# Optimization experiments

Hardware: AMD Instinct MI355X
Metric: run time of the kernel (lower is better)

## Reference

```python
import jax, jax.numpy as jnp
import numpy as np

B, D, L = 32, 512, 4096   # batch, latent_dim (dim1), time length
N, D2 = 77, 768           # text tokens, text_latent_dim (dim2)
BC = 24                   # number of conditioned batch elements
H = 8                     # num_heads
EPS = 1e-5


def _layernorm(x, g, b):
    mu = jnp.mean(x, axis=-1, keepdims=True)
    var = jnp.mean(jnp.square(x - mu), axis=-1, keepdims=True)
    return (x - mu) * jax.lax.rsqrt(var + EPS) * g + b


def setup_inputs() -> dict:
    key = jax.random.key(0)
    ks = jax.random.split(key, 8)
    s = 0.02
    return {
        "input_tensor": jax.random.normal(ks[0], (B, D, L), jnp.float32),
        "condition_tensor": jax.random.normal(ks[1], (B, N, D2), jnp.float32),
        "cond_indices": jnp.arange(BC, dtype=jnp.int64 if jax.config.jax_enable_x64 else jnp.int32),
        "ln_g": jnp.ones((D,), jnp.float32),
        "ln_b": jnp.zeros((D,), jnp.float32),
        "tln_g": jnp.ones((D2,), jnp.float32),
        "tln_b": jnp.zeros((D2,), jnp.float32),
        "Wq": jax.random.normal(ks[2], (D, D), jnp.float32) * s,
        "bq": jnp.zeros((D,), jnp.float32),
        "Wk": jax.random.normal(ks[3], (D2, D), jnp.float32) * s,
        "bk": jnp.zeros((D,), jnp.float32),
        "Wv": jax.random.normal(ks[4], (D2, D), jnp.float32) * s,
        "bv": jnp.zeros((D,), jnp.float32),
    }


def reference(input_tensor, condition_tensor, cond_indices,
              ln_g, ln_b, tln_g, tln_b, Wq, bq, Wk, bk, Wv, bv):
    dh = D // H
    # gather conditioned rows; [Bc, D, L] -> [Bc, T=L, D]
    x_cond = jnp.transpose(input_tensor[cond_indices], (0, 2, 1))
    cond = condition_tensor[cond_indices]  # [Bc, N, D2]

    q = _layernorm(x_cond, ln_g, ln_b) @ Wq + bq           # [Bc, T, D]
    cn = _layernorm(cond, tln_g, tln_b)                     # [Bc, N, D2]
    k = (cn @ Wk + bk).reshape(BC, N, H, dh)
    v = (cn @ Wv + bv).reshape(BC, N, H, dh)

    q = jax.nn.softmax(q.reshape(BC, L, H, dh), axis=-1)   # feature-map softmax
    k = jax.nn.softmax(k, axis=1)                           # softmax over tokens N

    context = jnp.einsum('bnhk,bnhv->bhkv', k, v)           # [Bc, H, dh, dh]
    y = jnp.einsum('bthk,bhkv->bthv', q, context).reshape(BC, L, D)

    # scatter residual back: indices are unique, so .add == torch index assignment
    return input_tensor.at[cond_indices].add(jnp.transpose(y, (0, 2, 1)))
```

## Files before the change

### kernel.cpp

```cpp
#include <hip/hip_runtime.h>
#include <hip/hip_bf16.h>

#define LN_EPS 1e-5f

typedef __attribute__((ext_vector_type(8))) short bf16x8;
typedef __attribute__((ext_vector_type(8))) short s16x8;
typedef __attribute__((ext_vector_type(4))) float f32x4;

__device__ __forceinline__ unsigned short f2bf(float f){
  unsigned u = __builtin_bit_cast(unsigned, f);
  u = (u + 0x7fffu + ((u >> 16) & 1u)) >> 16;
  return (unsigned short)u;
}
__device__ __forceinline__ void gll16(const void* g, void* l){
  __builtin_amdgcn_global_load_lds(
      (const __attribute__((address_space(1))) unsigned int*)(g),
      (__attribute__((address_space(3))) unsigned int*)(l), 16, 0, 0);
}

__global__ void k_wqt(const float* __restrict__ Wq, unsigned short* __restrict__ WqT){
  const int tid = blockIdx.x * 256 + threadIdx.x;
  const int d = tid >> 9, n = tid & 511;
  const int swz = (n >> 1) & 3;
  WqT[(size_t)n * 512 + (d ^ (swz << 3))] = f2bf(Wq[(size_t)d * 512 + n]);
}

__global__ void k_condkv(const float* __restrict__ cond, const int* __restrict__ idx,
                         const float* __restrict__ tg, const float* __restrict__ tb,
                         const float* __restrict__ Wk, const float* __restrict__ bk,
                         const float* __restrict__ Wv, const float* __restrict__ bv,
                         float* __restrict__ kbuf, float* __restrict__ vbuf)
{
  __shared__ float cn[16][768];
  const int bc = blockIdx.z, nc = blockIdx.y, dc = blockIdx.x;
  const int b = idx[bc];
  const int n0 = nc * 16;
  int nrows = 77 - n0; if(nrows > 16) nrows = 16;
  const int w = threadIdx.x >> 6, lane = threadIdx.x & 63;

  for(int r = w; r < nrows; r += 4){
    const float* src = cond + ((size_t)b * 77 + n0 + r) * 768;
    float vals[12]; float s1 = 0.f, s2 = 0.f;
    #pragma unroll
    for(int i=0;i<12;i++){ float x = src[lane + i*64]; vals[i]=x; s1+=x; s2+=x*x; }
    #pragma unroll
    for(int off=1; off<64; off<<=1){ s1 += __shfl_xor(s1, off); s2 += __shfl_xor(s2, off); }
    const float mu  = s1 * (1.f/768.f);
    const float var = s2 * (1.f/768.f) - mu*mu;
    const float rs  = rsqrtf(var + LN_EPS);
    #pragma unroll
    for(int i=0;i<12;i++){ const int c2 = lane + i*64; cn[r][c2] = (vals[i]-mu)*rs*tg[c2] + tb[c2]; }
  }
  __syncthreads();

  const int dq = threadIdx.x & 63;
  const int part = threadIdx.x >> 6;
  const float* W    = (dc < 2) ? Wk : Wv;
  const float* bias = (dc < 2) ? bk : bv;
  float* obuf       = (dc < 2) ? kbuf : vbuf;
  const int d0 = (dc & 1) * 256 + dq * 4;

  float acc[4][4] = {};
  for(int i=0;i<768;i++){
    const float4 wv = *(const float4*)(W + (size_t)i * 512 + d0);
    #pragma unroll
    for(int j=0;j<4;j++){
      const float c = cn[part*4 + j][i];
      acc[j][0] += c * wv.x; acc[j][1] += c * wv.y;
      acc[j][2] += c * wv.z; acc[j][3] += c * wv.w;
    }
  }
  #pragma unroll
  for(int j=0;j<4;j++){
    const int r = part*4 + j, n = n0 + r;
    if(r < nrows){
      float4 o;
      o.x = acc[j][0] + bias[d0+0];
      o.y = acc[j][1] + bias[d0+1];
      o.z = acc[j][2] + bias[d0+2];
      o.w = acc[j][3] + bias[d0+3];
      *(float4*)(obuf + ((size_t)bc * 77 + n) * 512 + d0) = o;
    }
  }
}

__global__ void k_ctx(const float* __restrict__ kbuf, const float* __restrict__ vbuf,
                      unsigned short* __restrict__ ctxP)
{
  __shared__ float kk[77][64];
  __shared__ float vv[77][64];
  __shared__ float inv_s[64];
  const int h = blockIdx.x, bc = blockIdx.y;
  const int tid = threadIdx.x;
  for(int e = tid; e < 77*64; e += 256){
    const int n = e >> 6, c = e & 63;
    kk[n][c] = kbuf[((size_t)bc * 77 + n) * 512 + h*64 + c];
    vv[n][c] = vbuf[((size_t)bc * 77 + n) * 512 + h*64 + c];
  }
  __syncthreads();
  if(tid < 64){
    float m = -1e30f;
    for(int n=0;n<77;n++) m = fmaxf(m, kk[n][tid]);
    float s = 0.f;
    for(int n=0;n<77;n++){ const float e = __expf(kk[n][tid] - m); kk[n][tid] = e; s += e; }
    inv_s[tid] = 1.f / s;
  }
  __syncthreads();
  #pragma unroll
  for(int j=0;j<16;j++){
    const int o = tid + 256*j;
    const int v = o >> 6, k2 = o & 63;
    float a = 0.f;
    for(int n=0;n<77;n++) a += kk[n][k2] * vv[n][v];
    const int pos = ((((k2>>5)*4 + (v>>4))*4 + ((k2>>3)&3))*16 + (v&15))*8 + (k2&7);
    ctxP[((size_t)(bc*8 + h)) * 4096 + pos] = f2bf(a * inv_s[k2]);
  }
}

__global__ void k_copy(const float* __restrict__ in, const int* __restrict__ idx,
                       float* __restrict__ out)
{
  const int b = blockIdx.y;
  bool member = false;
  for(int i=0;i<24;i++) member |= (idx[i] == b);
  if(member) return;
  const float4* s = (const float4*)(in  + (size_t)b * 512 * 4096);
  float4*       d = (float4*)      (out + (size_t)b * 512 * 4096);
  for(int i = blockIdx.x*256 + threadIdx.x; i < 512*4096/4; i += 128*256) d[i] = s[i];
}

__global__ __launch_bounds__(256, 2)
void k_lnt(const float* __restrict__ input, const int* __restrict__ idx,
           const float* __restrict__ ln_g, const float* __restrict__ ln_b,
           unsigned short* __restrict__ xT)
{
  __shared__ float buf[32][516];
  __shared__ float red1[32][8], red2[32][8];
  __shared__ float mu_s[32], rs_s[32];
  __shared__ float gbuf[512], bbuf[512];

  const int tid = threadIdx.x;
  const int bc = blockIdx.y;
  const int b  = idx[bc];
  const int t0 = blockIdx.x * 32;
  const float* xb = input + (size_t)b * (512*4096) + t0;

  *(float2*)&gbuf[tid*2] = *(const float2*)&ln_g[tid*2];
  *(float2*)&bbuf[tid*2] = *(const float2*)&ln_b[tid*2];

  {
    const int p  = tid & 7;
    const int dg = tid >> 3;
    #pragma unroll
    for(int i=0;i<16;i++){
      const int d = dg + i*32;
      const float4 x = *(const float4*)(xb + (size_t)d * 4096 + p*4);
      buf[p*4+0][d] = x.x; buf[p*4+1][d] = x.y;
      buf[p*4+2][d] = x.z; buf[p*4+3][d] = x.w;
    }
  }
  __syncthreads();

  {
    const int t = tid & 31, part = tid >> 5;
    float s1 = 0.f, s2 = 0.f;
    #pragma unroll
    for(int i=0;i<16;i++){
      const float4 v = *(const float4*)&buf[t][part*64 + i*4];
      s1 += v.x+v.y+v.z+v.w;
      s2 += v.x*v.x + v.y*v.y + v.z*v.z + v.w*v.w;
    }
    red1[t][part] = s1; red2[t][part] = s2;
  }
  __syncthreads();
  if(tid < 32){
    float a = 0.f, c = 0.f;
    #pragma unroll
    for(int p=0;p<8;p++){ a += red1[tid][p]; c += red2[tid][p]; }
    const float mu  = a * (1.f/512.f);
    const float var = c * (1.f/512.f) - mu*mu;
    mu_s[tid] = mu; rs_s[tid] = rsqrtf(var + LN_EPS);
  }
  __syncthreads();

  {
    const int c  = tid & 7;
    const int tt = tid >> 3;
    const float mu = mu_s[tt], rs = rs_s[tt];
    const int swz = (tt >> 1) & 3;
    unsigned short* orow = xT + ((size_t)bc*4096 + t0 + tt) * 512;
    #pragma unroll
    for(int j=0;j<8;j++){
      const int d0 = c*8 + j*64;
      const float4 a  = *(const float4*)&buf[tt][d0];
      const float4 b4 = *(const float4*)&buf[tt][d0+4];
      const float4 g0 = *(const float4*)&gbuf[d0];
      const float4 g1 = *(const float4*)&gbuf[d0+4];
      const float4 h0 = *(const float4*)&bbuf[d0];
      const float4 h1 = *(const float4*)&bbuf[d0+4];
      s16x8 o;
      o[0] = (short)f2bf((a.x -mu)*rs*g0.x + h0.x);
      o[1] = (short)f2bf((a.y -mu)*rs*g0.y + h0.y);
      o[2] = (short)f2bf((a.z -mu)*rs*g0.z + h0.z);
      o[3] = (short)f2bf((a.w -mu)*rs*g0.w + h0.w);
      o[4] = (short)f2bf((b4.x-mu)*rs*g1.x + h1.x);
      o[5] = (short)f2bf((b4.y-mu)*rs*g1.y + h1.y);
      o[6] = (short)f2bf((b4.z-mu)*rs*g1.z + h1.z);
      o[7] = (short)f2bf((b4.w-mu)*rs*g1.w + h1.w);
      *(s16x8*)(orow + (d0 ^ (swz << 3))) = o;
    }
  }
}

__global__ __launch_bounds__(256, 4)
void k_gemm3(const float* __restrict__ input, const int* __restrict__ idx,
             const unsigned short* __restrict__ xT, const unsigned short* __restrict__ WqT,
             const float* __restrict__ bq, const unsigned short* __restrict__ ctxP,
             float* __restrict__ out)
{
  __shared__ __align__(16) char smem[36864];
  char* Ab[2] = { smem,         smem + 16384 };
  char* Bb[2] = { smem + 8192,  smem + 24576 };
  unsigned short* P = (unsigned short*)smem;

  const int tid  = threadIdx.x;
  const int lane = tid & 63;
  const int w    = tid >> 6;
  const int col  = lane & 15;
  const int g    = lane >> 4;
  const int wm   = w >> 1, wn = w & 1;
  const int ntile = blockIdx.x, mtile = blockIdx.y;
  const int bc   = mtile >> 5;
  const int tt0  = (mtile & 31) * 128;
  const int b    = idx[bc];
  const int nbase = ntile * 128;
  const char* xTb = (const char*)xT + ((size_t)bc*4096 + tt0) * 1024;
  const char* wTb = (const char*)WqT + (size_t)nbase * 1024;

  const int f0 = tid * 16;
  const int f1 = f0 + 4096;
  const int r0 = f0 >> 6, o0 = f0 & 63;
  const int r1 = f1 >> 6, o1 = f1 & 63;

  #define STAGE(ks, bi)                                          \
  {                                                              \
    gll16(xTb + (size_t)r0*1024 + (ks)*64 + o0, Ab[bi] + f0);    \
    gll16(xTb + (size_t)r1*1024 + (ks)*64 + o1, Ab[bi] + f1);    \
    gll16(wTb + (size_t)r0*1024 + (ks)*64 + o0, Bb[bi] + f0);    \
    gll16(wTb + (size_t)r1*1024 + (ks)*64 + o1, Bb[bi] + f1);    \
  }

  f32x4 acc[4][4] = {};

  int offA[4], offB[4];
  #pragma unroll
  for(int mt=0; mt<4; ++mt){
    const int rowA = wm*64 + mt*16 + col;
    offA[mt] = rowA*64 + ((g ^ ((rowA>>1)&3)) << 4);
    const int rowB = wn*64 + mt*16 + col;
    offB[mt] = rowB*64 + ((g ^ ((rowB>>1)&3)) << 4);
  }

  STAGE(0, 0);
  asm volatile("s_waitcnt vmcnt(0)" ::: "memory");
  __builtin_amdgcn_s_barrier();

  for(int ks=0; ks<16; ++ks){
    const int cur = ks & 1;
    if(ks < 15) STAGE(ks+1, cur^1);

    bf16x8 af[4], bfr[4];
    #pragma unroll
    for(int mt=0; mt<4; ++mt) af[mt]  = *(const bf16x8*)(Ab[cur] + offA[mt]);
    #pragma unroll
    for(int nt=0; nt<4; ++nt) bfr[nt] = *(const bf16x8*)(Bb[cur] + offB[nt]);
    #pragma unroll
    for(int mt=0; mt<4; ++mt)
      #pragma unroll
      for(int nt=0; nt<4; ++nt)
        acc[mt][nt] = __builtin_amdgcn_mfma_f32_16x16x32_bf16(af[mt], bfr[nt], acc[mt][nt], 0, 0, 0);

    asm volatile("s_waitcnt vmcnt(0)" ::: "memory");
    __builtin_amdgcn_s_barrier();
  }
  #undef STAGE

  #pragma unroll
  for(int mt=0; mt<4; ++mt){
    #pragma unroll
    for(int nt=0; nt<4; ++nt){
      const float bqv = bq[nbase + wn*64 + nt*16 + col];
      #pragma unroll
      for(int r=0;r<4;++r) acc[mt][nt][r] += bqv;
    }
    #pragma unroll
    for(int r=0;r<4;++r){
      float m = fmaxf(fmaxf(acc[mt][0][r],acc[mt][1][r]), fmaxf(acc[mt][2][r],acc[mt][3][r]));
      m = fmaxf(m, __shfl_xor(m, 1));
      m = fmaxf(m, __shfl_xor(m, 2));
      m = fmaxf(m, __shfl_xor(m, 4));
      m = fmaxf(m, __shfl_xor(m, 8));
      float s = 0.f;
      #pragma unroll
      for(int q=0;q<4;++q){
        const float e = __expf(acc[mt][q][r] - m);
        acc[mt][q][r] = e; s += e;
      }
      s += __shfl_xor(s, 1);
      s += __shfl_xor(s, 2);
      s += __shfl_xor(s, 4);
      s += __shfl_xor(s, 8);
      const float inv = 1.f / s;
      #pragma unroll
      for(int q=0;q<4;++q) acc[mt][q][r] *= inv;
    }
  }

  unsigned short* Pw = P + w * 64 * 72;
  #pragma unroll
  for(int mt=0; mt<4; ++mt)
    #pragma unroll
    for(int nt=0; nt<4; ++nt)
      #pragma unroll
      for(int r=0; r<4; ++r)
        Pw[(mt*16 + g*4 + r)*72 + nt*16 + col] = f2bf(acc[mt][nt][r]);

  const int head = ntile*2 + wn;
  const unsigned short* cp = ctxP + (size_t)(bc*8 + head) * 4096;
  f32x4 y[4][4] = {};
  #pragma unroll
  for(int ks2=0; ks2<2; ++ks2){
    bf16x8 pa[4];
    #pragma unroll
    for(int mt=0; mt<4; ++mt)
      pa[mt] = *(const bf16x8*)(Pw + (mt*16 + col)*72 + ks2*32 + g*8);
    bf16x8 cv[4];
    #pragma unroll
    for(int vt=0; vt<4; ++vt)
      cv[vt] = *(const bf16x8*)(cp + (size_t)(((ks2*4 + vt)*4 + g)*16 + col) * 8);
    #pragma unroll
    for(int mt=0; mt<4; ++mt)
      #pragma unroll
      for(int vt=0; vt<4; ++vt)
        y[mt][vt] = __builtin_amdgcn_mfma_f32_16x16x32_bf16(pa[mt], cv[vt], y[mt][vt], 0, 0, 0);
  }

  const float* xb = input + (size_t)b * 512 * 4096;
  float*       ob = out   + (size_t)b * 512 * 4096;
  #pragma unroll
  for(int mt=0; mt<4; ++mt)
    #pragma unroll
    for(int vt=0; vt<4; ++vt){
      const size_t row = (size_t)(head*64 + vt*16 + col);
      const size_t a = row*4096 + (size_t)(tt0 + wm*64 + mt*16 + g*4);
      const float4 xr = *(const float4*)(xb + a);
      float4 o4;
      o4.x = xr.x + y[mt][vt][0];
      o4.y = xr.y + y[mt][vt][1];
      o4.z = xr.z + y[mt][vt][2];
      o4.w = xr.w + y[mt][vt][3];
      *(float4*)(ob + a) = o4;
    }
}

extern "C" void kernel_launch(void* const* d_in, const int* in_sizes, int n_in,
                              void* d_out, int out_size, void* d_ws, size_t ws_size,
                              hipStream_t stream)
{
  const float* input = (const float*)d_in[0];
  const float* cond  = (const float*)d_in[1];
  const int*   idx   = (const int*)d_in[2];
  const float* ln_g  = (const float*)d_in[3];
  const float* ln_b  = (const float*)d_in[4];
  const float* tln_g = (const float*)d_in[5];
  const float* tln_b = (const float*)d_in[6];
  const float* Wq    = (const float*)d_in[7];
  const float* bq    = (const float*)d_in[8];
  const float* Wk    = (const float*)d_in[9];
  const float* bk    = (const float*)d_in[10];
  const float* Wv    = (const float*)d_in[11];
  const float* bv    = (const float*)d_in[12];
  float* out = (float*)d_out;
  char*  ws  = (char*)d_ws;

  unsigned short* WqT  = (unsigned short*)(ws);
  unsigned short* ctxP = (unsigned short*)(ws + 524288);
  float* kbuf = (float*)(ws + 2097152);
  float* vbuf = (float*)(ws + 2097152 + 3784704);
  unsigned short* xT = (unsigned short*)(ws + 2097152 + 2*3784704);

  k_wqt   <<<dim3(1024),    dim3(256), 0, stream>>>(Wq, WqT);
  k_condkv<<<dim3(4,5,24),  dim3(256), 0, stream>>>(cond, idx, tln_g, tln_b, Wk, bk, Wv, bv, kbuf, vbuf);
  k_ctx   <<<dim3(8,24),    dim3(256), 0, stream>>>(kbuf, vbuf, ctxP);
  k_copy  <<<dim3(128,32),  dim3(256), 0, stream>>>(input, idx, out);
  k_lnt   <<<dim3(128,24),  dim3(256), 0, stream>>>(input, idx, ln_g, ln_b, xT);
  k_gemm3 <<<dim3(4,768),   dim3(256), 0, stream>>>(input, idx, xT, WqT, bq, ctxP, out);
}
```

Baseline: 446.3 us.

## Merge auxiliary kernels and triple-buffer GEMM K-loop with prefetch depth two

Folds the Wq transpose into the cond K/V projection kernel as an extra grid slice, and folds the passthrough copy of unconditioned batches into the layernorm-transpose kernel. This cuts the number of launches from six to four. The Q GEMM now uses three LDS stages with two K-steps in flight, waiting with vmcnt(4) instead of draining all loads each step. LDS per block grows to 48KB and occupancy bounds drop from 4 to 3 blocks, which could reduce latency hiding elsewhere.

```diff
diff --git a/kernel.cpp b/kernel.cpp
--- a/kernel.cpp
+++ b/kernel.cpp
@@ -1,5 +1,4 @@
 #include <hip/hip_runtime.h>
-#include <hip/hip_bf16.h>
 
 #define LN_EPS 1e-5f
 
@@ -18,25 +17,41 @@
       (__attribute__((address_space(3))) unsigned int*)(l), 16, 0, 0);
 }
 
-__global__ void k_wqt(const float* __restrict__ Wq, unsigned short* __restrict__ WqT){
-  const int tid = blockIdx.x * 256 + threadIdx.x;
-  const int d = tid >> 9, n = tid & 511;
-  const int swz = (n >> 1) & 3;
-  WqT[(size_t)n * 512 + (d ^ (swz << 3))] = f2bf(Wq[(size_t)d * 512 + n]);
-}
-
-__global__ void k_condkv(const float* __restrict__ cond, const int* __restrict__ idx,
-                         const float* __restrict__ tg, const float* __restrict__ tb,
-                         const float* __restrict__ Wk, const float* __restrict__ bk,
-                         const float* __restrict__ Wv, const float* __restrict__ bv,
-                         float* __restrict__ kbuf, float* __restrict__ vbuf)
+__global__ void k_aux(const float* __restrict__ Wq,
+                      unsigned short* __restrict__ WqT,
+                      const float* __restrict__ cond, const int* __restrict__ idx,
+                      const float* __restrict__ tg, const float* __restrict__ tb,
+                      const float* __restrict__ Wk, const float* __restrict__ bk,
+                      const float* __restrict__ Wv, const float* __restrict__ bv,
+                      float* __restrict__ kbuf, float* __restrict__ vbuf)
 {
   __shared__ float cn[16][768];
+  const int tid = threadIdx.x;
+
+  if(blockIdx.z == 24){
+    const int pb = blockIdx.x + 4*blockIdx.y;
+    if(pb >= 16) return;
+    const int c = tid & 31, q = tid >> 5;
+    const int n = pb*32 + c;
+    const int swz = (n >> 1) & 3;
+    for(int i=0;i<64;i+=4){
+      ushort4 pkv;
+      unsigned short* pp = (unsigned short*)&pkv;
+      #pragma unroll
+      for(int j=0;j<4;j++){
+        const int d = q*64 + i + j;
+        pp[j] = f2bf(Wq[(size_t)d*512 + n]);
+      }
+      *(ushort4*)(WqT + (size_t)n*512 + ((q*64 + i) ^ (swz << 3))) = pkv;
+    }
+    return;
+  }
+
   const int bc = blockIdx.z, nc = blockIdx.y, dc = blockIdx.x;
   const int b = idx[bc];
   const int n0 = nc * 16;
   int nrows = 77 - n0; if(nrows > 16) nrows = 16;
-  const int w = threadIdx.x >> 6, lane = threadIdx.x & 63;
+  const int w = tid >> 6, lane = tid & 63;
 
   for(int r = w; r < nrows; r += 4){
     const float* src = cond + ((size_t)b * 77 + n0 + r) * 768;
@@ -53,8 +68,8 @@
   }
   __syncthreads();
 
-  const int dq = threadIdx.x & 63;
-  const int part = threadIdx.x >> 6;
+  const int dq = tid & 63;
+  const int part = tid >> 6;
   const float* W    = (dc < 2) ? Wk : Wv;
   const float* bias = (dc < 2) ? bk : bv;
   float* obuf       = (dc < 2) ? kbuf : vbuf;
@@ -117,22 +132,10 @@
   }
 }
 
-__global__ void k_copy(const float* __restrict__ in, const int* __restrict__ idx,
-                       float* __restrict__ out)
-{
-  const int b = blockIdx.y;
-  bool member = false;
-  for(int i=0;i<24;i++) member |= (idx[i] == b);
-  if(member) return;
-  const float4* s = (const float4*)(in  + (size_t)b * 512 * 4096);
-  float4*       d = (float4*)      (out + (size_t)b * 512 * 4096);
-  for(int i = blockIdx.x*256 + threadIdx.x; i < 512*4096/4; i += 128*256) d[i] = s[i];
-}
-
 __global__ __launch_bounds__(256, 2)
 void k_lnt(const float* __restrict__ input, const int* __restrict__ idx,
            const float* __restrict__ ln_g, const float* __restrict__ ln_b,
-           unsigned short* __restrict__ xT)
+           unsigned short* __restrict__ xT, float* __restrict__ out)
 {
   __shared__ float buf[32][516];
   __shared__ float red1[32][8], red2[32][8];
@@ -140,6 +143,23 @@
   __shared__ float gbuf[512], bbuf[512];
 
   const int tid = threadIdx.x;
+
+  if(blockIdx.y >= 24){
+    const int nb = blockIdx.y - 24;
+    int cnt = 0, bsel = 0;
+    for(int b2 = 0; b2 < 32; ++b2){
+      bool member = false;
+      #pragma unroll
+      for(int i2 = 0; i2 < 24; ++i2) member |= (idx[i2] == b2);
+      if(!member){ if(cnt == nb) bsel = b2; ++cnt; }
+    }
+    const float4* s = (const float4*)(input + (size_t)bsel * 2097152) + (size_t)blockIdx.x * 4096;
+    float4*       d = (float4*)      (out   + (size_t)bsel * 2097152) + (size_t)blockIdx.x * 4096;
+    #pragma unroll
+    for(int i = 0; i < 16; ++i) d[i*256 + tid] = s[i*256 + tid];
+    return;
+  }
+
   const int bc = blockIdx.y;
   const int b  = idx[bc];
   const int t0 = blockIdx.x * 32;
@@ -212,15 +232,13 @@
   }
 }
 
-__global__ __launch_bounds__(256, 4)
+__global__ __launch_bounds__(256, 3)
 void k_gemm3(const float* __restrict__ input, const int* __restrict__ idx,
              const unsigned short* __restrict__ xT, const unsigned short* __restrict__ WqT,
              const float* __restrict__ bq, const unsigned short* __restrict__ ctxP,
              float* __restrict__ out)
 {
-  __shared__ __align__(16) char smem[36864];
-  char* Ab[2] = { smem,         smem + 16384 };
-  char* Bb[2] = { smem + 8192,  smem + 24576 };
+  __shared__ __align__(16) char smem[49152];
   unsigned short* P = (unsigned short*)smem;
 
   const int tid  = threadIdx.x;
@@ -242,12 +260,13 @@
   const int r0 = f0 >> 6, o0 = f0 & 63;
   const int r1 = f1 >> 6, o1 = f1 & 63;
 
-  #define STAGE(ks, bi)                                          \
-  {                                                              \
-    gll16(xTb + (size_t)r0*1024 + (ks)*64 + o0, Ab[bi] + f0);    \
-    gll16(xTb + (size_t)r1*1024 + (ks)*64 + o1, Ab[bi] + f1);    \
-    gll16(wTb + (size_t)r0*1024 + (ks)*64 + o0, Bb[bi] + f0);    \
-    gll16(wTb + (size_t)r1*1024 + (ks)*64 + o1, Bb[bi] + f1);    \
+  #define STAGE(ks, bi)                                                   \
+  {                                                                       \
+    char* dst = smem + (bi)*16384;                                        \
+    gll16(xTb + (size_t)r0*1024 + (ks)*64 + o0, dst + f0);                \
+    gll16(xTb + (size_t)r1*1024 + (ks)*64 + o1, dst + f1);                \
+    gll16(wTb + (size_t)r0*1024 + (ks)*64 + o0, dst + 8192 + f0);         \
+    gll16(wTb + (size_t)r1*1024 + (ks)*64 + o1, dst + 8192 + f1);         \
   }
 
   f32x4 acc[4][4] = {};
@@ -262,28 +281,29 @@
   }
 
   STAGE(0, 0);
-  asm volatile("s_waitcnt vmcnt(0)" ::: "memory");
-  __builtin_amdgcn_s_barrier();
-
+  STAGE(1, 1);
+
+  #pragma unroll
   for(int ks=0; ks<16; ++ks){
-    const int cur = ks & 1;
-    if(ks < 15) STAGE(ks+1, cur^1);
-
+    if(ks < 15) asm volatile("s_waitcnt vmcnt(4)" ::: "memory");
+    else        asm volatile("s_waitcnt vmcnt(0)" ::: "memory");
+    __builtin_amdgcn_s_barrier();
+    if(ks < 14) STAGE(ks+2, (ks+2)%3);
+
+    char* cur = smem + (ks%3)*16384;
     bf16x8 af[4], bfr[4];
     #pragma unroll
-    for(int mt=0; mt<4; ++mt) af[mt]  = *(const bf16x8*)(Ab[cur] + offA[mt]);
-    #pragma unroll
-    for(int nt=0; nt<4; ++nt) bfr[nt] = *(const bf16x8*)(Bb[cur] + offB[nt]);
+    for(int mt=0; mt<4; ++mt) af[mt]  = *(const bf16x8*)(cur + offA[mt]);
+    #pragma unroll
+    for(int nt=0; nt<4; ++nt) bfr[nt] = *(const bf16x8*)(cur + 8192 + offB[nt]);
     #pragma unroll
     for(int mt=0; mt<4; ++mt)
       #pragma unroll
       for(int nt=0; nt<4; ++nt)
         acc[mt][nt] = __builtin_amdgcn_mfma_f32_16x16x32_bf16(af[mt], bfr[nt], acc[mt][nt], 0, 0, 0);
-
-    asm volatile("s_waitcnt vmcnt(0)" ::: "memory");
-    __builtin_amdgcn_s_barrier();
   }
   #undef STAGE
+  __syncthreads();
 
   #pragma unroll
   for(int mt=0; mt<4; ++mt){
@@ -345,14 +365,14 @@
         y[mt][vt] = __builtin_amdgcn_mfma_f32_16x16x32_bf16(pa[mt], cv[vt], y[mt][vt], 0, 0, 0);
   }
 
-  const float* xb = input + (size_t)b * 512 * 4096;
-  float*       ob = out   + (size_t)b * 512 * 4096;
+  const float* xb = input + (size_t)b * 2097152;
+  float*       ob = out   + (size_t)b * 2097152;
   #pragma unroll
   for(int mt=0; mt<4; ++mt)
     #pragma unroll
     for(int vt=0; vt<4; ++vt){
-      const size_t row = (size_t)(head*64 + vt*16 + col);
-      const size_t a = row*4096 + (size_t)(tt0 + wm*64 + mt*16 + g*4);
+      const size_t a = (size_t)(head*64 + vt*16 + col)*4096
+                     + (size_t)(tt0 + wm*64 + mt*16 + g*4);
       const float4 xr = *(const float4*)(xb + a);
       float4 o4;
       o4.x = xr.x + y[mt][vt][0];
@@ -389,10 +409,9 @@
   float* vbuf = (float*)(ws + 2097152 + 3784704);
   unsigned short* xT = (unsigned short*)(ws + 2097152 + 2*3784704);
 
-  k_wqt   <<<dim3(1024),    dim3(256), 0, stream>>>(Wq, WqT);
-  k_condkv<<<dim3(4,5,24),  dim3(256), 0, stream>>>(cond, idx, tln_g, tln_b, Wk, bk, Wv, bv, kbuf, vbuf);
-  k_ctx   <<<dim3(8,24),    dim3(256), 0, stream>>>(kbuf, vbuf, ctxP);
-  k_copy  <<<dim3(128,32),  dim3(256), 0, stream>>>(input, idx, out);
-  k_lnt   <<<dim3(128,24),  dim3(256), 0, stream>>>(input, idx, ln_g, ln_b, xT);
-  k_gemm3 <<<dim3(4,768),   dim3(256), 0, stream>>>(input, idx, xT, WqT, bq, ctxP, out);
-}
+  k_aux  <<<dim3(4,5,25),  dim3(256), 0, stream>>>(Wq, WqT, cond, idx, tln_g, tln_b,
+                                                   Wk, bk, Wv, bv, kbuf, vbuf);
+  k_ctx  <<<dim3(8,24),    dim3(256), 0, stream>>>(kbuf, vbuf, ctxP);
+  k_lnt  <<<dim3(128,32),  dim3(256), 0, stream>>>(input, idx, ln_g, ln_b, xT, out);
+  k_gemm3<<<dim3(4,768),   dim3(256), 0, stream>>>(input, idx, xT, WqT, bq, ctxP, out);
+}
```

After: 449.0 us. Within noise of the previous version (+0.6%).
